# Optimization experiments

Hardware: AMD Instinct MI355X
Metric: run time of the kernel (lower is better)

Reference implementation:

```python
import jax, jax.numpy as jnp
import numpy as np

N_NODES = 100000
N_EDGES = 1600000
IN_F, OUT_F = 25, 50


def setup_inputs() -> dict:
    key = jax.random.key(0)
    k1, k2, k3, k4 = jax.random.split(key, 4)
    x = jax.random.normal(k1, (N_NODES, IN_F), dtype=jnp.float32)
    W = jax.random.normal(k2, (IN_F, OUT_F), dtype=jnp.float32) * (1.0 / np.sqrt(IN_F))
    b = jax.random.normal(k3, (OUT_F,), dtype=jnp.float32) * 0.01
    edge_index = jax.random.randint(k4, (2, N_EDGES), 0, N_NODES, dtype=jnp.int64)
    return {"x": x, "W": W, "b": b, "edge_index": edge_index}


def reference(x, W, b, edge_index):
    # GCNConv(normalize=False): linear transform, then add-aggregate over edges, + bias.
    src, dst = edge_index[0], edge_index[1]
    h = x @ W                                   # [N, OUT_F] small dense GEMM
    msgs = h[src]                               # [E, OUT_F] irregular gather
    agg = jax.ops.segment_sum(msgs, dst, num_segments=N_NODES)  # scatter-add to targets
    out = agg + b
    return jax.nn.relu(out)
```

## Files before the change

### kernel.cpp

```cpp
#include <hip/hip_runtime.h>

#define N_NODES 100000
#define N_EDGES 1600000
#define IN_F 25
#define OUT_F 50

#define BNODES 98
#define NBUCK 1024
#define DL_SHIFT 7
#define SLAB 1920
#define BIN_NB 98
#define BIN_CHUNK 16384
#define XPREP_ITEMS (N_NODES * 16)
#define PREP_GRID 512

__global__ __launch_bounds__(1024) void gcn_prep_kernel(
        const float* __restrict__ x,
        const int* __restrict__ ei,
        int* __restrict__ gfill,
        unsigned* __restrict__ recs,
        unsigned* __restrict__ xb) {
    __shared__ int lcnt[NBUCK];
    __shared__ int lbase[NBUCK];
    int tid = threadIdx.x, bid = blockIdx.x;
    if (bid < BIN_NB) {
        for (int i = tid; i < NBUCK; i += 1024) lcnt[i] = 0;
        __syncthreads();
        const int4* s4 = (const int4*)ei;
        const int4* d4 = (const int4*)(ei + N_EDGES);
        int base4 = bid * (BIN_CHUNK / 4);
        int4 sv[4], dv[4];
        bool ok[4];
#pragma unroll
        for (int k = 0; k < 4; ++k) {
            int i4 = base4 + k * 1024 + tid;
            ok[k] = (i4 < N_EDGES / 4);
            if (ok[k]) { dv[k] = d4[i4]; sv[k] = s4[i4]; }
        }
#pragma unroll
        for (int k = 0; k < 4; ++k) {
            if (ok[k]) {
                const int* dd = &dv[k].x;
#pragma unroll
                for (int c = 0; c < 4; ++c)
                    atomicAdd(&lcnt[((unsigned)dd[c]) / BNODES], 1);
            }
        }
        __syncthreads();
        for (int i = tid; i < NBUCK; i += 1024) {
            int c = lcnt[i];
            lbase[i] = c ? atomicAdd(&gfill[i], c) : 0;
            lcnt[i] = 0;
        }
        __syncthreads();
#pragma unroll
        for (int k = 0; k < 4; ++k) {
            if (ok[k]) {
                const int* dd = &dv[k].x;
                const int* ss = &sv[k].x;
#pragma unroll
                for (int c = 0; c < 4; ++c) {
                    unsigned d = (unsigned)dd[c], s = (unsigned)ss[c];
                    unsigned bk = d / BNODES;
                    unsigned dl = d - bk * BNODES;
                    int p = lbase[bk] + atomicAdd(&lcnt[bk], 1);
                    if ((unsigned)p < SLAB)
                        recs[bk * SLAB + p] = (s << DL_SHIFT) | dl;
                }
            }
        }
    } else {
        for (int idx = (bid - BIN_NB) * 1024 + tid; idx < XPREP_ITEMS;
             idx += (PREP_GRID - BIN_NB) * 1024) {
            int n  = idx >> 4;
            int fp = (idx & 15) * 2;
            float v0 = (fp < IN_F) ? x[n * IN_F + fp] : 0.f;
            float v1 = (fp + 1 < IN_F) ? x[n * IN_F + fp + 1] : 0.f;
            union { float fl; unsigned u; } a, c;
            a.fl = v0; c.fl = v1;
            unsigned r0 = (a.u + 0x7FFFu + ((a.u >> 16) & 1u)) >> 16;
            unsigned r1 = (c.u + 0x7FFFu + ((c.u >> 16) & 1u)) >> 16;
            xb[idx] = (r1 << 16) | (r0 & 0xFFFFu);
        }
    }
}

__global__ __launch_bounds__(512, 8) void gcn_k3_kernel(
        const uint4* __restrict__ xb4,
        const unsigned* __restrict__ recs,
        const int* __restrict__ gfill,
        const float* __restrict__ W,
        const float* __restrict__ b,
        float* __restrict__ out) {
    __shared__ unsigned raw[SLAB];
    __shared__ int      srt[SLAB];
    __shared__ int      cnt[128], fil[128];
    __shared__ int      offs[BNODES + 1];
    __shared__ float    acc[BNODES * IN_F];
    __shared__ float    Ws[IN_F * OUT_F];
    __shared__ float    bs[OUT_F];

    int bk = blockIdx.x, tid = threadIdx.x;
    if (tid < 128) { cnt[tid] = 0; fil[tid] = 0; }
    for (int i = tid; i < IN_F * OUT_F; i += 512) Ws[i] = W[i];
    if (tid < OUT_F) bs[tid] = b[tid];
    __syncthreads();

    int cntE = min(gfill[bk], SLAB);
    const unsigned* rb = recs + bk * SLAB;

    for (int j = tid; j < cntE; j += 512) {
        unsigned rec = rb[j];
        raw[j] = rec;
        atomicAdd(&cnt[rec & ((1 << DL_SHIFT) - 1)], 1);
    }
    __syncthreads();

    if (tid < 64) {
        int v = cnt[tid];
        for (int off = 1; off < 64; off <<= 1) {
            int t = __shfl_up(v, off, 64);
            if (tid >= off) v += t;
        }
        offs[tid + 1] = v;
        int t64 = __shfl(v, 63, 64);
        int v2 = (tid < BNODES - 64) ? cnt[64 + tid] : 0;
        for (int off = 1; off < 64; off <<= 1) {
            int t = __shfl_up(v2, off, 64);
            if (tid >= off) v2 += t;
        }
        if (tid < BNODES - 64) offs[65 + tid] = t64 + v2;
        if (tid == 0) offs[0] = 0;
    }
    __syncthreads();

    for (int j = tid; j < cntE; j += 512) {
        unsigned rec = raw[j];
        int dl = rec & ((1 << DL_SHIFT) - 1);
        int p = offs[dl] + atomicAdd(&fil[dl], 1);
        srt[p] = (int)(rec >> DL_SHIFT);
    }
    __syncthreads();

    {
        int g = tid >> 2, f = tid & 3;
        if (g < BNODES) {
            int e0 = offs[g], e1 = offs[g + 1];
            float a0 = 0.f, a1 = 0.f, a2 = 0.f, a3 = 0.f;
            float a4 = 0.f, a5 = 0.f, a6 = 0.f, a7 = 0.f;
            int j = e0;
            for (; j + 4 <= e1; j += 4) {
                uint4 u[4];
#pragma unroll
                for (int q = 0; q < 4; ++q) u[q] = xb4[srt[j + q] * 4 + f];
#pragma unroll
                for (int q = 0; q < 4; ++q) {
                    union { unsigned uu; float fl; } t0, t1, t2, t3, t4, t5, t6, t7;
                    t0.uu = u[q].x << 16; t1.uu = u[q].x & 0xFFFF0000u;
                    t2.uu = u[q].y << 16; t3.uu = u[q].y & 0xFFFF0000u;
                    t4.uu = u[q].z << 16; t5.uu = u[q].z & 0xFFFF0000u;
                    t6.uu = u[q].w << 16; t7.uu = u[q].w & 0xFFFF0000u;
                    a0 += t0.fl; a1 += t1.fl; a2 += t2.fl; a3 += t3.fl;
                    a4 += t4.fl; a5 += t5.fl; a6 += t6.fl; a7 += t7.fl;
                }
            }
            for (; j < e1; ++j) {
                uint4 u = xb4[srt[j] * 4 + f];
                union { unsigned uu; float fl; } t0, t1, t2, t3, t4, t5, t6, t7;
                t0.uu = u.x << 16; t1.uu = u.x & 0xFFFF0000u;
                t2.uu = u.y << 16; t3.uu = u.y & 0xFFFF0000u;
                t4.uu = u.z << 16; t5.uu = u.z & 0xFFFF0000u;
                t6.uu = u.w << 16; t7.uu = u.w & 0xFFFF0000u;
                a0 += t0.fl; a1 += t1.fl; a2 += t2.fl; a3 += t3.fl;
                a4 += t4.fl; a5 += t5.fl; a6 += t6.fl; a7 += t7.fl;
            }
            int ff = 8 * f;
            float av[8] = {a0, a1, a2, a3, a4, a5, a6, a7};
#pragma unroll
            for (int k = 0; k < 8; ++k)
                if (ff + k < IN_F) acc[g * IN_F + ff + k] = av[k];
        }
    }
    __syncthreads();

    int node0 = bk * BNODES;
    for (int i = tid; i < BNODES * OUT_F; i += 512) {
        int nl = i / OUT_F;
        int o  = i - nl * OUT_F;
        int node = node0 + nl;
        if (node < N_NODES) {
            float a = bs[o];
#pragma unroll
            for (int k = 0; k < IN_F; ++k)
                a += acc[nl * IN_F + k] * Ws[k * OUT_F + o];
            out[node * OUT_F + o] = fmaxf(a, 0.f);
        }
    }
}

extern "C" void kernel_launch(void* const* d_in, const int* in_sizes, int n_in,
                              void* d_out, int out_size, void* d_ws, size_t ws_size,
                              hipStream_t stream) {
    const float* x  = (const float*)d_in[0];
    const float* W  = (const float*)d_in[1];
    const float* b  = (const float*)d_in[2];
    const int*   ei = (const int*)d_in[3];
    float* out = (float*)d_out;

    char* ws = (char*)d_ws;
    unsigned* xb    = (unsigned*)(ws);
    unsigned* recs  = (unsigned*)(ws + 6400000);
    int*      gfill = (int*)(ws + 14264576);

    hipMemsetAsync(gfill, 0, NBUCK * sizeof(int), stream);
    gcn_prep_kernel<<<PREP_GRID, 1024, 0, stream>>>(x, ei, gfill, recs, xb);
    gcn_k3_kernel<<<NBUCK, 512, 0, stream>>>((const uint4*)xb, recs, gfill, W, b, out);
}
```

Before: 128.9 us.

## Split bucket slabs into two halves and pad transposed W for the GEMM

The binning blocks now alternate between two global fill counters and two half-slabs per bucket, keyed by block parity, which halves contention on each global atomic counter. The aggregation kernel reads both halves and joins them. The epilogue GEMM also stores W transposed with a padded stride of 28, alongside padded accumulator rows, so each thread reads contiguous rows. This changes the LDS bank access pattern. Overflow capacity per half is now 1024, so a skewed split between the halves could drop edges that the old single 1920 slab would have kept.

```diff
diff --git a/kernel.cpp b/kernel.cpp
--- a/kernel.cpp
+++ b/kernel.cpp
@@ -8,7 +8,9 @@
 #define BNODES 98
 #define NBUCK 1024
 #define DL_SHIFT 7
-#define SLAB 1920
+#define SLABH 1024
+#define SLAB 2048
+#define ACCP 28
 #define BIN_NB 98
 #define BIN_CHUNK 16384
 #define XPREP_ITEMS (N_NODES * 16)
@@ -24,6 +26,8 @@
     __shared__ int lbase[NBUCK];
     int tid = threadIdx.x, bid = blockIdx.x;
     if (bid < BIN_NB) {
+        int r = bid & 1;
+        int rOff = r * SLABH;
         for (int i = tid; i < NBUCK; i += 1024) lcnt[i] = 0;
         __syncthreads();
         const int4* s4 = (const int4*)ei;
@@ -49,7 +53,7 @@
         __syncthreads();
         for (int i = tid; i < NBUCK; i += 1024) {
             int c = lcnt[i];
-            lbase[i] = c ? atomicAdd(&gfill[i], c) : 0;
+            lbase[i] = c ? atomicAdd(&gfill[r * NBUCK + i], c) : 0;
             lcnt[i] = 0;
         }
         __syncthreads();
@@ -64,8 +68,8 @@
                     unsigned bk = d / BNODES;
                     unsigned dl = d - bk * BNODES;
                     int p = lbase[bk] + atomicAdd(&lcnt[bk], 1);
-                    if ((unsigned)p < SLAB)
-                        recs[bk * SLAB + p] = (s << DL_SHIFT) | dl;
+                    if ((unsigned)p < SLABH)
+                        recs[bk * SLAB + rOff + p] = (s << DL_SHIFT) | dl;
                 }
             }
         }
@@ -96,21 +100,26 @@
     __shared__ int      srt[SLAB];
     __shared__ int      cnt[128], fil[128];
     __shared__ int      offs[BNODES + 1];
-    __shared__ float    acc[BNODES * IN_F];
-    __shared__ float    Ws[IN_F * OUT_F];
+    __shared__ float    acc[BNODES * ACCP];
+    __shared__ float    Wt[OUT_F * ACCP];
     __shared__ float    bs[OUT_F];
 
     int bk = blockIdx.x, tid = threadIdx.x;
     if (tid < 128) { cnt[tid] = 0; fil[tid] = 0; }
-    for (int i = tid; i < IN_F * OUT_F; i += 512) Ws[i] = W[i];
+    for (int i = tid; i < OUT_F * IN_F; i += 512) {
+        int o = i / IN_F, k = i - o * IN_F;
+        Wt[o * ACCP + k] = W[k * OUT_F + o];
+    }
     if (tid < OUT_F) bs[tid] = b[tid];
     __syncthreads();
 
-    int cntE = min(gfill[bk], SLAB);
+    int c0 = min(gfill[bk], SLABH);
+    int c1 = min(gfill[NBUCK + bk], SLABH);
+    int cntE = c0 + c1;
     const unsigned* rb = recs + bk * SLAB;
 
     for (int j = tid; j < cntE; j += 512) {
-        unsigned rec = rb[j];
+        unsigned rec = (j < c0) ? rb[j] : rb[SLABH + (j - c0)];
         raw[j] = rec;
         atomicAdd(&cnt[rec & ((1 << DL_SHIFT) - 1)], 1);
     }
@@ -178,7 +187,7 @@
             float av[8] = {a0, a1, a2, a3, a4, a5, a6, a7};
 #pragma unroll
             for (int k = 0; k < 8; ++k)
-                if (ff + k < IN_F) acc[g * IN_F + ff + k] = av[k];
+                if (ff + k < IN_F) acc[g * ACCP + ff + k] = av[k];
         }
     }
     __syncthreads();
@@ -189,10 +198,12 @@
         int o  = i - nl * OUT_F;
         int node = node0 + nl;
         if (node < N_NODES) {
+            const float* ar = &acc[nl * ACCP];
+            const float* wr = &Wt[o * ACCP];
             float a = bs[o];
 #pragma unroll
             for (int k = 0; k < IN_F; ++k)
-                a += acc[nl * IN_F + k] * Ws[k * OUT_F + o];
+                a += ar[k] * wr[k];
             out[node * OUT_F + o] = fmaxf(a, 0.f);
         }
     }
@@ -210,9 +221,9 @@
     char* ws = (char*)d_ws;
     unsigned* xb    = (unsigned*)(ws);
     unsigned* recs  = (unsigned*)(ws + 6400000);
-    int*      gfill = (int*)(ws + 14264576);
-
-    hipMemsetAsync(gfill, 0, NBUCK * sizeof(int), stream);
+    int*      gfill = (int*)(ws + 14788608);
+
+    hipMemsetAsync(gfill, 0, 2 * NBUCK * sizeof(int), stream);
     gcn_prep_kernel<<<PREP_GRID, 1024, 0, stream>>>(x, ei, gfill, recs, xb);
     gcn_k3_kernel<<<NBUCK, 512, 0, stream>>>((const uint4*)xb, recs, gfill, W, b, out);
 }
```

Result: slower. 132.0 us (+2.4%).
